# Kernel optimization log

Measured on AMD Instinct MI355X. Metric: run time of the kernel, lower is better.

The kernel has to match this reference:

```python
import jax, jax.numpy as jnp
import numpy as np

D_MODEL = 1024
NUM_HEADS = 16
D_FF = 4096
SEQ = 2048
BATCH = 2
THETA = 10000.0
EPS = 1e-5


def _param(key, shape, fan_in, fan_out):
    std = 2.0 / (fan_in + fan_out) ** 0.5
    return std * jax.random.truncated_normal(key, -3.0, 3.0, shape, dtype=jnp.float32)


def setup_inputs() -> dict:
    key = jax.random.key(0)
    ks = jax.random.split(key, 8)
    d, h, f = D_MODEL, NUM_HEADS, D_FF
    return {
        'x': jax.random.normal(ks[0], (BATCH, SEQ, d), dtype=jnp.float32),
        'token_positions': jnp.arange(SEQ, dtype=jnp.int32),
        'wq': _param(ks[1], (d, d), d, d),
        'wk': _param(ks[2], (d, d), d, d),
        'wv': _param(ks[3], (d, d), d, d),
        'wo': _param(ks[4], (d, d), d, d),
        'ln1_w': jnp.ones((d,), jnp.float32),
        'ln2_w': jnp.ones((d,), jnp.float32),
        'w1': _param(ks[5], (f, d), d, f),
        'w2': _param(ks[6], (d, f), f, d),
        'w3': _param(ks[7], (f, d), d, f),
    }


def rmsnorm(x, w):
    x32 = x.astype(jnp.float32)
    rms = jnp.sqrt(jnp.mean(x32 * x32, axis=-1, keepdims=True) + EPS)
    return ((x32 / rms) * w).astype(x.dtype)


def apply_rope(x, cos, sin):
    # x: [b, h, s, d_k]; cos/sin: [s, d_k//2] -> broadcast as [1,1,s,d_k//2]
    xe, xo = x[..., ::2], x[..., 1::2]
    c = cos[None, None, :, :]
    s = sin[None, None, :, :]
    re = xe * c - xo * s
    ro = xe * s + xo * c
    return jnp.stack((re, ro), axis=-1).reshape(x.shape)


def block_forward(x, token_positions, wq, wk, wv, wo, ln1_w, ln2_w, w1, w2, w3):
    b, s, d = x.shape
    h = NUM_HEADS
    dk = d // h
    # RoPE tables at token positions
    inv_freq = 1.0 / (THETA ** (jnp.arange(0, dk // 2, dtype=jnp.float32) * 2.0 / dk))
    freqs = token_positions.astype(jnp.float32)[:, None] * inv_freq[None, :]  # [s, dk/2]
    cos, sin = jnp.cos(freqs), jnp.sin(freqs)

    # --- attention sublayer (pre-norm) ---
    xn = rmsnorm(x, ln1_w)
    q = jnp.einsum('bsd,ed->bse', xn, wq).reshape(b, s, h, dk).transpose(0, 2, 1, 3)
    k = jnp.einsum('bsd,ed->bse', xn, wk).reshape(b, s, h, dk).transpose(0, 2, 1, 3)
    v = jnp.einsum('bsd,ed->bse', xn, wv).reshape(b, s, h, dk).transpose(0, 2, 1, 3)
    q = apply_rope(q, cos, sin)
    k = apply_rope(k, cos, sin)
    scores = jnp.einsum('bhqd,bhkd->bhqk', q, k) / jnp.sqrt(jnp.float32(dk))
    causal = jnp.tril(jnp.ones((s, s), dtype=bool))
    scores = jnp.where(causal[None, None], scores, -jnp.inf)
    attn = jax.nn.softmax(scores, axis=-1)
    o = jnp.einsum('bhqk,bhkd->bhqd', attn, v)
    o = o.transpose(0, 2, 1, 3).reshape(b, s, d)
    x = x + jnp.einsum('bse,de->bsd', o, wo)

    # --- SwiGLU sublayer (pre-norm) ---
    xn = rmsnorm(x, ln2_w)
    x1 = jnp.einsum('bsd,fd->bsf', xn, w1)
    x3 = jnp.einsum('bsd,fd->bsf', xn, w3)
    gated = (x1 * jax.nn.sigmoid(x1)) * x3
    return x + jnp.einsum('bsf,df->bsd', gated, w2)


def reference(x, token_positions, wq, wk, wv, wo, ln1_w, ln2_w, w1, w2, w3):
    return block_forward(x, token_positions, wq, wk, wv, wo, ln1_w, ln2_w, w1, w2, w3)
```

## Files before the change

### kernel.cpp

```cpp
#include <hip/hip_runtime.h>
#include <hip/hip_bf16.h>

typedef __attribute__((ext_vector_type(4))) float f32x4;
typedef __attribute__((ext_vector_type(8))) short bf16x8;
typedef unsigned short u16;
typedef unsigned int u32;
typedef __attribute__((ext_vector_type(4))) u16 u16x4;

#define DEV static __device__ __forceinline__

constexpr int Bb = 2, Ss = 2048, Dd = 1024, Hh = 16, DKk = 64;
constexpr int Mm = Bb * Ss;

DEV float bf2f(u16 u) { union { u32 i; float f; } v; v.i = (u32)u << 16; return v.f; }
DEV u16 f2bf(float f) {
  union { float f; u32 i; } v; v.f = f;
  u32 r = v.i + 0x7FFFu + ((v.i >> 16) & 1u);
  return (u16)(r >> 16);
}

DEV void gload_lds16(const u16* g, u16* l) {
  __builtin_amdgcn_global_load_lds((const __attribute__((address_space(1))) u32*)g,
                                   (__attribute__((address_space(3))) u32*)l, 16, 0, 0);
}

DEV int swz16(int o) {
  return o ^ (((o >> 8) & 1) << 6) ^ (((o >> 9) & 1) << 5);
}

__global__ void k_cvt_all(const float* __restrict__ wq, const float* __restrict__ wk,
                          const float* __restrict__ wv, const float* __restrict__ wo,
                          const float* __restrict__ w1, const float* __restrict__ w2,
                          const float* __restrict__ w3,
                          u16* __restrict__ wqkv, u16* __restrict__ wob,
                          u16* __restrict__ w13, u16* __restrict__ w2b) {
  int i = (blockIdx.x * 256 + threadIdx.x) * 4;
  int seg = i >> 20;
  const float* src; u16* dst;
  if (seg == 0)      { src = wq + i;             dst = wqkv + i; }
  else if (seg == 1) { src = wk + (i - (1<<20)); dst = wqkv + i; }
  else if (seg == 2) { src = wv + (i - (2<<20)); dst = wqkv + i; }
  else if (seg == 3) { src = wo + (i - (3<<20)); dst = wob  + (i - (3<<20)); }
  else if (seg < 8)  { src = w1 + (i - (4<<20)); dst = w13  + (i - (4<<20)); }
  else if (seg < 12) { src = w2 + (i - (8<<20)); dst = w2b  + (i - (8<<20)); }
  else               { src = w3 + (i - (12<<20)); dst = w13 + (4<<20) + (i - (12<<20)); }
  float4 v = *(const float4*)src;
  u16x4 o = { f2bf(v.x), f2bf(v.y), f2bf(v.z), f2bf(v.w) };
  *(u16x4*)dst = o;
}

__global__ __launch_bounds__(256) void k_rmsnorm(const float* __restrict__ x,
                                                 const float* __restrict__ w,
                                                 u16* __restrict__ out) {
  int row = blockIdx.x;
  int t = threadIdx.x;
  float4 v = ((const float4*)(x + (long)row * Dd))[t];
  float ss = v.x * v.x + v.y * v.y + v.z * v.z + v.w * v.w;
#pragma unroll
  for (int m = 32; m; m >>= 1) ss += __shfl_xor(ss, m, 64);
  __shared__ float red[4];
  if ((t & 63) == 0) red[t >> 6] = ss;
  __syncthreads();
  float tot = red[0] + red[1] + red[2] + red[3];
  float r = rsqrtf(tot * (1.0f / Dd) + 1e-5f);
  float4 wv = ((const float4*)w)[t];
  u16x4 o = { f2bf(v.x * r * wv.x), f2bf(v.y * r * wv.y),
              f2bf(v.z * r * wv.z), f2bf(v.w * r * wv.w) };
  ((u16x4*)(out + (long)row * Dd))[t] = o;
}

__global__ void k_rope(u16* __restrict__ q, u16* __restrict__ k, const int* __restrict__ tp) {
  int idx = blockIdx.x * 256 + threadIdx.x;
  if (idx >= Bb * Ss * Hh * 32) return;
  int p = idx & 31;
  int h = (idx >> 5) & 15;
  int row = idx >> 9;
  int s = row & (Ss - 1);
  float pos = (float)tp[s];
  float invf = __expf(-(float)p * (2.0f / DKk) * 9.2103403719761836f);
  float fr = pos * invf;
  float sn, cs;
  sincosf(fr, &sn, &cs);
  long base = (long)row * Dd + h * DKk + 2 * p;
  float xe = bf2f(q[base]), xo = bf2f(q[base + 1]);
  q[base]     = f2bf((xe * cs - xo * sn) * 0.125f);
  q[base + 1] = f2bf((xe * sn + xo * cs) * 0.125f);
  xe = bf2f(k[base]); xo = bf2f(k[base + 1]);
  k[base]     = f2bf(xe * cs - xo * sn);
  k[base + 1] = f2bf(xe * sn + xo * cs);
}

template <int OM, bool RES>
__global__ __launch_bounds__(256) void k_gemm(const u16* __restrict__ A,
                                              const u16* __restrict__ Bm,
                                              void* __restrict__ Cout,
                                              const float* __restrict__ Rres,
                                              int N, int K) {
  __shared__ u16 Abuf[128 * 32];
  __shared__ u16 Bbuf[128 * 32];
  const int tid = threadIdx.x;
  const int wid = tid >> 6, lane = tid & 63;
  const int wm = wid >> 1, wn = wid & 1;
  const int lq = lane >> 4, ll = lane & 15;
  const int lin = blockIdx.y * gridDim.x + blockIdx.x;
  const int c = lin & 7, j = lin >> 3;
  const int ncc = gridDim.x >> 2;
  const int bxc = (c % ncc) * 4 + (j & 3);
  const int byc = (c / ncc) * 8 + (j >> 2);
  const int m0 = byc * 128, n0 = bxc * 128;

  f32x4 acc[4][4] = {};

  const int srow = tid >> 2;
  const int scol = (tid & 3) * 8;
  const long aoff = (long)(m0 + srow) * K + scol;
  const long boff = (long)(n0 + srow) * K + scol;
  u16* aldsw = Abuf + wid * 512;
  u16* bldsw = Bbuf + wid * 512;

  for (int k0 = 0; k0 < K; k0 += 32) {
    __syncthreads();
    gload_lds16(A + aoff + k0, aldsw);
    gload_lds16(A + aoff + (long)64 * K + k0, aldsw + 2048);
    gload_lds16(Bm + boff + k0, bldsw);
    gload_lds16(Bm + boff + (long)64 * K + k0, bldsw + 2048);
    __syncthreads();
    bf16x8 af[4], bfr[4];
#pragma unroll
    for (int i = 0; i < 4; i++)
      af[i] = *(const bf16x8*)&Abuf[(wm * 64 + i * 16 + ll) * 32 + lq * 8];
#pragma unroll
    for (int j2 = 0; j2 < 4; j2++)
      bfr[j2] = *(const bf16x8*)&Bbuf[(wn * 64 + j2 * 16 + ll) * 32 + lq * 8];
#pragma unroll
    for (int i = 0; i < 4; i++)
#pragma unroll
      for (int j2 = 0; j2 < 4; j2++)
        acc[i][j2] = __builtin_amdgcn_mfma_f32_16x16x32_bf16(af[i], bfr[j2], acc[i][j2], 0, 0, 0);
  }

#pragma unroll
  for (int i = 0; i < 4; i++) {
    const int rowb = m0 + wm * 64 + i * 16 + lq * 4;
#pragma unroll
    for (int j2 = 0; j2 < 4; j2++) {
      const int col = n0 + wn * 64 + j2 * 16 + ll;
#pragma unroll
      for (int r = 0; r < 4; r++) {
        int rr = rowb + r;
        float v = acc[i][j2][r];
        if (RES) v += Rres[(long)rr * N + col];
        if (OM == 1) {
          ((float*)Cout)[(long)rr * N + col] = v;
        } else {
          ((u16*)Cout)[(long)rr * N + col] = f2bf(v);
        }
      }
    }
  }
}

#define STG_A(d, h, kt)                                                         \
  { gload_lds16(A + aoff[0] + (long)(h) * 128 * K + (kt) * 64, &sA[d][h][dst0]); \
    gload_lds16(A + aoff[1] + (long)(h) * 128 * K + (kt) * 64, &sA[d][h][dst1]); }
#define STG_B(d, h, kt)                                                         \
  { gload_lds16(Bp + boff[0] + (long)(h) * 128 * K + (kt) * 64, &sB[d][h][dst0]); \
    gload_lds16(Bp + boff[1] + (long)(h) * 128 * K + (kt) * 64, &sB[d][h][dst1]); }

#define PHASE(q, d, DOB, WVN, ...)                                              \
  {                                                                             \
    bf16x8 af_[2][2];                                                           \
    _Pragma("unroll") for (int s_ = 0; s_ < 2; s_++)                            \
    _Pragma("unroll") for (int kk_ = 0; kk_ < 2; kk_++) {                       \
      int ms_ = (q) * 4 + wm * 2 + s_;                                          \
      int lo_ = ((ms_ & 7) * 16 + ll) * 128 + kk_ * 64 + lq * 16;               \
      af_[s_][kk_] = *(const bf16x8*)((const char*)sA[d][ms_ >> 3] + swz16(lo_)); \
    }                                                                           \
    if (DOB) {                                                                  \
      _Pragma("unroll") for (int ns_ = 0; ns_ < 4; ns_++)                       \
      _Pragma("unroll") for (int kk_ = 0; kk_ < 2; kk_++) {                     \
        int rl_ = wn * 64 + ns_ * 16 + ll;                                      \
        int lo_ = (rl_ & 127) * 128 + kk_ * 64 + lq * 16;                       \
        bfr[ns_][kk_] = *(const bf16x8*)((const char*)sB[d][rl_ >> 7] + swz16(lo_)); \
      }                                                                         \
    }                                                                           \
    __VA_ARGS__;                                                                \
    __builtin_amdgcn_s_barrier();                                               \
    asm volatile("s_waitcnt lgkmcnt(0)" ::: "memory");                          \
    __builtin_amdgcn_sched_barrier(0);                                          \
    __builtin_amdgcn_s_setprio(1);                                              \
    _Pragma("unroll") for (int s_ = 0; s_ < 2; s_++)                            \
    _Pragma("unroll") for (int ns_ = 0; ns_ < 4; ns_++)                         \
    _Pragma("unroll") for (int kk_ = 0; kk_ < 2; kk_++)                         \
      acc[q][s_][ns_] = __builtin_amdgcn_mfma_f32_16x16x32_bf16(                \
          af_[s_][kk_], bfr[ns_][kk_], acc[q][s_][ns_], 0, 0, 0);               \
    __builtin_amdgcn_s_setprio(0);                                              \
    { int wv_ = (WVN);                                                          \
      if (wv_ == 6) { asm volatile("s_waitcnt vmcnt(6)" ::: "memory"); }        \
      else if (wv_ == 0) { asm volatile("s_waitcnt vmcnt(0)" ::: "memory"); } } \
    __builtin_amdgcn_s_barrier();                                               \
  }

template <int OM, int CW, int CH>
__global__ __launch_bounds__(512) void k_gemm8(const u16* __restrict__ A,
                                               const u16* __restrict__ Bm,
                                               void* __restrict__ Cout,
                                               int N, int K) {
  __shared__ u16 sA[2][2][8192];
  __shared__ u16 sB[2][2][8192];
  const int gx = gridDim.x;
  const int lin = blockIdx.y * gx + blockIdx.x;
  const int c = lin & 7, j = lin >> 3;
  const int ncc = gx / CW;
  const int bx = (c % ncc) * CW + j % CW;
  const int by = (c / ncc) * CH + j / CW;
  const long m0 = (long)by * 256, n0 = (long)bx * 256;
  const int tid = threadIdx.x;
  const int wid = tid >> 6, lane = tid & 63;
  const int wm = wid >> 2, wn = wid & 3;
  const int lq = lane >> 4, ll = lane & 15;

  long aoff[2], boff[2];
#pragma unroll
  for (int j2 = 0; j2 < 2; j2++) {
    int off = j2 * 8192 + wid * 1024 + lane * 16;
    int lo = swz16(off);
    int r = lo >> 7, cc = (lo & 127) >> 1;
    aoff[j2] = (m0 + r) * K + cc;
    boff[j2] = (n0 + r) * K + cc;
  }
  const int dst0 = wid * 512;
  const int dst1 = 4096 + wid * 512;

  f32x4 acc[4][2][4];
  bf16x8 bfr[4][2];
  u32 stash[4][2][4][2];

  const int NT = K >> 6;
  const int NI = NT >> 1;
  constexpr int REPS = (OM == 5) ? 2 : 1;

  for (int rep = 0; rep < REPS; rep++) {
    const u16* Bp = Bm + (long)rep * 4096 * K;
    const f32x4 zz = {0.f, 0.f, 0.f, 0.f};
#pragma unroll
    for (int q = 0; q < 4; q++)
#pragma unroll
      for (int s = 0; s < 2; s++)
#pragma unroll
        for (int ns = 0; ns < 4; ns++) acc[q][s][ns] = zz;

    STG_A(0, 0, 0); STG_A(0, 1, 0); STG_B(0, 0, 0); STG_B(0, 1, 0);
    STG_B(1, 0, 1); STG_B(1, 1, 1); STG_A(1, 0, 1);
    asm volatile("s_waitcnt vmcnt(6)" ::: "memory");
    __builtin_amdgcn_s_barrier();

    for (int it = 0; it < NI; it++) {
      const int t = 2 * it;
      const bool full = (t + 2 < NT);
      PHASE(0, 0, true,  -1,            STG_A(1, 1, t + 1))
      PHASE(1, 0, false, -1,            if (full) STG_B(0, 0, t + 2))
      PHASE(2, 0, false, -1,            if (full) STG_B(0, 1, t + 2))
      PHASE(3, 0, false, full ? 6 : 0,  if (full) STG_A(0, 0, t + 2))
      PHASE(0, 1, true,  -1,            if (full) STG_A(0, 1, t + 2))
      PHASE(1, 1, false, -1,            if (full) STG_B(1, 0, t + 3))
      PHASE(2, 1, false, -1,            if (full) STG_B(1, 1, t + 3))
      PHASE(3, 1, false, full ? 6 : -1, if (full) STG_A(1, 0, t + 3))
    }

    if (OM == 5 && rep == 0) {
#pragma unroll
      for (int q = 0; q < 4; q++)
#pragma unroll
        for (int s = 0; s < 2; s++)
#pragma unroll
          for (int ns = 0; ns < 4; ns++) {
            stash[q][s][ns][0] = (u32)f2bf(acc[q][s][ns][0]) | ((u32)f2bf(acc[q][s][ns][1]) << 16);
            stash[q][s][ns][1] = (u32)f2bf(acc[q][s][ns][2]) | ((u32)f2bf(acc[q][s][ns][3]) << 16);
          }
    }
  }

#pragma unroll
  for (int q = 0; q < 4; q++)
#pragma unroll
    for (int s = 0; s < 2; s++) {
      const long row0 = m0 + (q * 4 + wm * 2 + s) * 16 + lq * 4;
#pragma unroll
      for (int ns = 0; ns < 4; ns++) {
        const long col = n0 + wn * 64 + ns * 16 + ll;
#pragma unroll
        for (int r = 0; r < 4; r++) {
          long rr = row0 + r;
          if (OM == 3) {
            float v = acc[q][s][ns][r];
            if (col < 2048) {
              ((u16*)Cout)[(col >> 10) * (long)(Mm * 1024) + rr * 1024 + (col & 1023)] = f2bf(v);
            } else {
              int d = col & 63, hh = ((int)col >> 6) & 15;
              int b2 = (int)rr >> 11, s2 = (int)rr & (Ss - 1);
              ((u16*)Cout)[(long)(2 * Mm * 1024) + ((long)((b2 * Hh + hh) * DKk + d)) * Ss + s2] = f2bf(v);
            }
          } else {
            float v3 = acc[q][s][ns][r];
            u32 st = stash[q][s][ns][r >> 1];
            u16 bb = (r & 1) ? (u16)(st >> 16) : (u16)(st & 0xffffu);
            float v1 = bf2f(bb);
            float g = v1 / (1.0f + __expf(-v1)) * v3;
            ((u16*)Cout)[rr * 4096 + col] = f2bf(g);
          }
        }
      }
    }
}

constexpr int PPAD = 80;

DEV void attn_tile(const u16* __restrict__ Kc, const u16* __restrict__ Vc,
                   u16* __restrict__ myP, const bf16x8* qf, f32x4* accO,
                   float* mrow, float* lrow, int qloc, bool diag, int lq, int ll) {
  f32x4 sacc[4] = {};
#pragma unroll
  for (int fn = 0; fn < 4; fn++)
#pragma unroll
    for (int ks = 0; ks < 2; ks++) {
      bf16x8 kf = *(const bf16x8*)&Kc[(fn * 16 + ll) * 64 + (((ks * 4 + lq) ^ (ll & 7)) * 8)];
      sacc[fn] = __builtin_amdgcn_mfma_f32_16x16x32_bf16(qf[ks], kf, sacc[fn], 0, 0, 0);
    }
  float sv[4][4], pmax[4];
#pragma unroll
  for (int r = 0; r < 4; r++) pmax[r] = -1e30f;
#pragma unroll
  for (int fn = 0; fn < 4; fn++) {
    int kc = fn * 16 + ll;
#pragma unroll
    for (int r = 0; r < 4; r++) {
      float v = sacc[fn][r];
      if (diag && kc > qloc + r) v = -1e30f;
      sv[fn][r] = v;
      pmax[r] = fmaxf(pmax[r], v);
    }
  }
#pragma unroll
  for (int r = 0; r < 4; r++) {
#pragma unroll
    for (int m = 1; m < 16; m <<= 1) pmax[r] = fmaxf(pmax[r], __shfl_xor(pmax[r], m, 64));
  }
  float alpha[4], rsum[4];
#pragma unroll
  for (int r = 0; r < 4; r++) {
    float mnew = fmaxf(mrow[r], pmax[r]);
    alpha[r] = __expf(mrow[r] - mnew);
    mrow[r] = mnew;
    rsum[r] = 0.f;
  }
#pragma unroll
  for (int fn = 0; fn < 4; fn++) {
#pragma unroll
    for (int r = 0; r < 4; r++) {
      float p = __expf(sv[fn][r] - mrow[r]);
      rsum[r] += p;
      myP[(lq * 4 + r) * PPAD + fn * 16 + ll] = f2bf(p);
    }
  }
#pragma unroll
  for (int r = 0; r < 4; r++) {
#pragma unroll
    for (int m = 1; m < 16; m <<= 1) rsum[r] += __shfl_xor(rsum[r], m, 64);
    lrow[r] = lrow[r] * alpha[r] + rsum[r];
  }
#pragma unroll
  for (int fn = 0; fn < 4; fn++)
#pragma unroll
    for (int r = 0; r < 4; r++) accO[fn][r] *= alpha[r];
  bf16x8 pa[2];
#pragma unroll
  for (int ks = 0; ks < 2; ks++)
    pa[ks] = *(const bf16x8*)&myP[ll * PPAD + ks * 32 + lq * 8];
#pragma unroll
  for (int fn = 0; fn < 4; fn++)
#pragma unroll
    for (int ks = 0; ks < 2; ks++) {
      bf16x8 vf = *(const bf16x8*)&Vc[(fn * 16 + ll) * 64 + (((ks * 4 + lq) ^ (ll & 7)) * 8)];
      accO[fn] = __builtin_amdgcn_mfma_f32_16x16x32_bf16(pa[ks], vf, accO[fn], 0, 0, 0);
    }
}

__global__ __launch_bounds__(256) void k_attn(const u16* __restrict__ Q,
                                              const u16* __restrict__ Kb,
                                              const u16* __restrict__ VT,
                                              u16* __restrict__ O) {
  __shared__ u16 Kt[2][64 * 64];
  __shared__ u16 Vt[2][64 * 64];
  __shared__ u16 P[4][16 * PPAD];
  const int pair = blockIdx.x;
  const int bh = blockIdx.y;
  const int b = bh >> 4, h = bh & 15;
  const int tid = threadIdx.x;
  const int wid = tid >> 6, lane = tid & 63;
  const int lq = lane >> 4, ll = lane & 15;
  const int qtA = pair, qtB = 31 - pair;
  const int qr0A = qtA * 64 + wid * 16;
  const int qr0B = qtB * 64 + wid * 16;
  const int qloc = wid * 16 + lq * 4;
  const long qkbase = ((long)b * Ss) * Dd + h * DKk;
  const long vbase  = ((long)(b * Hh + h) * DKk) * Ss;
  const int nk = 32 - pair;

  const int slot0 = wid * 64 + lane;
  const int r0 = slot0 >> 3, c0 = (slot0 & 7) ^ (r0 & 7);
  const int slot1 = 256 + slot0;
  const int r1 = slot1 >> 3, c1 = (slot1 & 7) ^ (r1 & 7);
  const int ldsb0 = (wid * 64) * 8;
  const int ldsb1 = (256 + wid * 64) * 8;

  bf16x8 qfA[2], qfB[2];
#pragma unroll
  for (int ks = 0; ks < 2; ks++) {
    qfA[ks] = *(const bf16x8*)&Q[qkbase + (long)(qr0A + ll) * Dd + ks * 32 + lq * 8];
    qfB[ks] = *(const bf16x8*)&Q[qkbase + (long)(qr0B + ll) * Dd + ks * 32 + lq * 8];
  }

  f32x4 accA[4] = {}, accB[4] = {};
  float mA[4], lA[4], mB[4], lB[4];
#pragma unroll
  for (int r = 0; r < 4; r++) { mA[r] = mB[r] = -1e30f; lA[r] = lB[r] = 0.f; }
  u16* myP = P[wid];

  gload_lds16(Kb + qkbase + (long)r0 * Dd + c0 * 8, Kt[0] + ldsb0);
  gload_lds16(Kb + qkbase + (long)r1 * Dd + c1 * 8, Kt[0] + ldsb1);
  gload_lds16(VT + vbase + (long)r0 * Ss + c0 * 8, Vt[0] + ldsb0);
  gload_lds16(VT + vbase + (long)r1 * Ss + c1 * 8, Vt[0] + ldsb1);
  __syncthreads();

  for (int kt = 0; kt < nk; kt++) {
    if (kt + 1 < nk) {
      const int kn = (kt + 1) * 64;
      u16* kd = Kt[(kt + 1) & 1];
      u16* vd = Vt[(kt + 1) & 1];
      gload_lds16(Kb + qkbase + (long)(kn + r0) * Dd + c0 * 8, kd + ldsb0);
      gload_lds16(Kb + qkbase + (long)(kn + r1) * Dd + c1 * 8, kd + ldsb1);
      gload_lds16(VT + vbase + (long)r0 * Ss + kn + c0 * 8, vd + ldsb0);
      gload_lds16(VT + vbase + (long)r1 * Ss + kn + c1 * 8, vd + ldsb1);
    }
    const u16* Kc = Kt[kt & 1];
    const u16* Vc = Vt[kt & 1];

    attn_tile(Kc, Vc, myP, qfB, accB, mB, lB, qloc, kt == nk - 1, lq, ll);
    if (kt <= pair)
      attn_tile(Kc, Vc, myP, qfA, accA, mA, lA, qloc, kt == pair, lq, ll);
    __syncthreads();
  }

#pragma unroll
  for (int fn = 0; fn < 4; fn++) {
#pragma unroll
    for (int r = 0; r < 4; r++) {
      int rowA = qr0A + lq * 4 + r;
      int rowB = qr0B + lq * 4 + r;
      O[((long)(b * Ss + rowA)) * Dd + h * DKk + fn * 16 + ll] = f2bf(accA[fn][r] / lA[r]);
      O[((long)(b * Ss + rowB)) * Dd + h * DKk + fn * 16 + ll] = f2bf(accB[fn][r] / lB[r]);
    }
  }
}

extern "C" void kernel_launch(void* const* d_in, const int* in_sizes, int n_in,
                              void* d_out, int out_size, void* d_ws, size_t ws_size,
                              hipStream_t stream) {
  const float* x   = (const float*)d_in[0];
  const int*   tp  = (const int*)d_in[1];
  const float* wq  = (const float*)d_in[2];
  const float* wk  = (const float*)d_in[3];
  const float* wv  = (const float*)d_in[4];
  const float* wo  = (const float*)d_in[5];
  const float* ln1 = (const float*)d_in[6];
  const float* ln2 = (const float*)d_in[7];
  const float* w1  = (const float*)d_in[8];
  const float* w2  = (const float*)d_in[9];
  const float* w3  = (const float*)d_in[10];

  char* ws = (char*)d_ws;
  const size_t MB = 1024 * 1024;
  u16*   wqkv_b = (u16*)(ws + 0 * MB);
  u16*   wo_b   = (u16*)(ws + 6 * MB);
  u16*   w13_b  = (u16*)(ws + 8 * MB);
  u16*   w2_b   = (u16*)(ws + 24 * MB);
  u16*   xn     = (u16*)(ws + 32 * MB);
  float* x2     = (float*)(ws + 40 * MB);
  u16*   qb     = (u16*)(ws + 56 * MB);
  u16*   kb     = (u16*)(ws + 64 * MB);
  u16*   vtb    = (u16*)(ws + 72 * MB);
  u16*   ob     = (u16*)(ws + 80 * MB);
  u16*   x1     = (u16*)(ws + 56 * MB);

  k_cvt_all<<<16384, 256, 0, stream>>>(wq, wk, wv, wo, w1, w2, w3,
                                       wqkv_b, wo_b, w13_b, w2_b);
  k_rmsnorm<<<Mm, 256, 0, stream>>>(x, ln1, xn);
  k_gemm8<3, 6, 4><<<dim3(12, 16), 512, 0, stream>>>(xn, wqkv_b, qb, 3072, 1024);
  k_rope<<<(Bb * Ss * Hh * 32) / 256, 256, 0, stream>>>(qb, kb, tp);
  k_attn<<<dim3(16, 32), 256, 0, stream>>>(qb, kb, vtb, ob);
  k_gemm<1, true><<<dim3(8, 32), 256, 0, stream>>>(ob, wo_b, x2, x, 1024, 1024);
  k_rmsnorm<<<Mm, 256, 0, stream>>>(x2, ln2, xn);
  k_gemm8<5, 4, 8><<<dim3(16, 16), 512, 0, stream>>>(xn, w13_b, x1, 4096, 1024);
  k_gemm<1, true><<<dim3(8, 32), 256, 0, stream>>>(x1, w2_b, (float*)d_out, x2, 1024, 4096);
}
```

Before: 380.4 us.

## Unfuse SwiGLU gate from W1/W3 GEMM and split-K the W2 GEMM

```diff
diff --git a/kernel.cpp b/kernel.cpp
--- a/kernel.cpp
+++ b/kernel.cpp
@@ -90,12 +90,36 @@
   k[base + 1] = f2bf(xe * sn + xo * cs);
 }
 
+__global__ void k_gate(u16* __restrict__ x1, const u16* __restrict__ x3, int n) {
+  int i = (blockIdx.x * 256 + threadIdx.x) * 4;
+  if (i >= n) return;
+  u16x4 a = *(u16x4*)(x1 + i);
+  u16x4 b = *(const u16x4*)(x3 + i);
+#pragma unroll
+  for (int j = 0; j < 4; j++) {
+    float v = bf2f(a[j]);
+    float g = v / (1.0f + __expf(-v)) * bf2f(b[j]);
+    a[j] = f2bf(g);
+  }
+  *(u16x4*)(x1 + i) = a;
+}
+
+__global__ void k_addout(const float* __restrict__ p0, const float* __restrict__ p1,
+                         const float* __restrict__ x2, float* __restrict__ out) {
+  int i = (blockIdx.x * 256 + threadIdx.x) * 4;
+  float4 a = *(const float4*)(p0 + i);
+  float4 b = *(const float4*)(p1 + i);
+  float4 c = *(const float4*)(x2 + i);
+  float4 o = { a.x + b.x + c.x, a.y + b.y + c.y, a.z + b.z + c.z, a.w + b.w + c.w };
+  *(float4*)(out + i) = o;
+}
+
 template <int OM, bool RES>
 __global__ __launch_bounds__(256) void k_gemm(const u16* __restrict__ A,
                                               const u16* __restrict__ Bm,
                                               void* __restrict__ Cout,
                                               const float* __restrict__ Rres,
-                                              int N, int K) {
+                                              int N, int Kl, int Kstr) {
   __shared__ u16 Abuf[128 * 32];
   __shared__ u16 Bbuf[128 * 32];
   const int tid = threadIdx.x;
@@ -109,21 +133,24 @@
   const int byc = (c / ncc) * 8 + (j >> 2);
   const int m0 = byc * 128, n0 = bxc * 128;
 
+  const u16* Ap = A + (long)blockIdx.z * Kl;
+  const u16* Bp = Bm + (long)blockIdx.z * Kl;
+
   f32x4 acc[4][4] = {};
 
   const int srow = tid >> 2;
   const int scol = (tid & 3) * 8;
-  const long aoff = (long)(m0 + srow) * K + scol;
-  const long boff = (long)(n0 + srow) * K + scol;
+  const long aoff = (long)(m0 + srow) * Kstr + scol;
+  const long boff = (long)(n0 + srow) * Kstr + scol;
   u16* aldsw = Abuf + wid * 512;
   u16* bldsw = Bbuf + wid * 512;
 
-  for (int k0 = 0; k0 < K; k0 += 32) {
+  for (int k0 = 0; k0 < Kl; k0 += 32) {
     __syncthreads();
-    gload_lds16(A + aoff + k0, aldsw);
-    gload_lds16(A + aoff + (long)64 * K + k0, aldsw + 2048);
-    gload_lds16(Bm + boff + k0, bldsw);
-    gload_lds16(Bm + boff + (long)64 * K + k0, bldsw + 2048);
+    gload_lds16(Ap + aoff + k0, aldsw);
+    gload_lds16(Ap + aoff + (long)64 * Kstr + k0, aldsw + 2048);
+    gload_lds16(Bp + boff + k0, bldsw);
+    gload_lds16(Bp + boff + (long)64 * Kstr + k0, bldsw + 2048);
     __syncthreads();
     bf16x8 af[4], bfr[4];
 #pragma unroll
@@ -139,6 +166,7 @@
         acc[i][j2] = __builtin_amdgcn_mfma_f32_16x16x32_bf16(af[i], bfr[j2], acc[i][j2], 0, 0, 0);
   }
 
+  float* fout = (float*)Cout + (long)blockIdx.z * Mm * (long)N;
 #pragma unroll
   for (int i = 0; i < 4; i++) {
     const int rowb = m0 + wm * 64 + i * 16 + lq * 4;
@@ -151,7 +179,7 @@
         float v = acc[i][j2][r];
         if (RES) v += Rres[(long)rr * N + col];
         if (OM == 1) {
-          ((float*)Cout)[(long)rr * N + col] = v;
+          fout[(long)rr * N + col] = v;
         } else {
           ((u16*)Cout)[(long)rr * N + col] = f2bf(v);
         }
@@ -164,8 +192,8 @@
   { gload_lds16(A + aoff[0] + (long)(h) * 128 * K + (kt) * 64, &sA[d][h][dst0]); \
     gload_lds16(A + aoff[1] + (long)(h) * 128 * K + (kt) * 64, &sA[d][h][dst1]); }
 #define STG_B(d, h, kt)                                                         \
-  { gload_lds16(Bp + boff[0] + (long)(h) * 128 * K + (kt) * 64, &sB[d][h][dst0]); \
-    gload_lds16(Bp + boff[1] + (long)(h) * 128 * K + (kt) * 64, &sB[d][h][dst1]); }
+  { gload_lds16(Bm + boff[0] + (long)(h) * 128 * K + (kt) * 64, &sB[d][h][dst0]); \
+    gload_lds16(Bm + boff[1] + (long)(h) * 128 * K + (kt) * 64, &sB[d][h][dst1]); }
 
 #define PHASE(q, d, DOB, WVN, ...)                                              \
   {                                                                             \
@@ -232,53 +260,28 @@
   const int dst0 = wid * 512;
   const int dst1 = 4096 + wid * 512;
 
-  f32x4 acc[4][2][4];
+  f32x4 acc[4][2][4] = {};
   bf16x8 bfr[4][2];
-  u32 stash[4][2][4][2];
 
   const int NT = K >> 6;
   const int NI = NT >> 1;
-  constexpr int REPS = (OM == 5) ? 2 : 1;
-
-  for (int rep = 0; rep < REPS; rep++) {
-    const u16* Bp = Bm + (long)rep * 4096 * K;
-    const f32x4 zz = {0.f, 0.f, 0.f, 0.f};
-#pragma unroll
-    for (int q = 0; q < 4; q++)
-#pragma unroll
-      for (int s = 0; s < 2; s++)
-#pragma unroll
-        for (int ns = 0; ns < 4; ns++) acc[q][s][ns] = zz;
-
-    STG_A(0, 0, 0); STG_A(0, 1, 0); STG_B(0, 0, 0); STG_B(0, 1, 0);
-    STG_B(1, 0, 1); STG_B(1, 1, 1); STG_A(1, 0, 1);
-    asm volatile("s_waitcnt vmcnt(6)" ::: "memory");
-    __builtin_amdgcn_s_barrier();
-
-    for (int it = 0; it < NI; it++) {
-      const int t = 2 * it;
-      const bool full = (t + 2 < NT);
-      PHASE(0, 0, true,  -1,            STG_A(1, 1, t + 1))
-      PHASE(1, 0, false, -1,            if (full) STG_B(0, 0, t + 2))
-      PHASE(2, 0, false, -1,            if (full) STG_B(0, 1, t + 2))
-      PHASE(3, 0, false, full ? 6 : 0,  if (full) STG_A(0, 0, t + 2))
-      PHASE(0, 1, true,  -1,            if (full) STG_A(0, 1, t + 2))
-      PHASE(1, 1, false, -1,            if (full) STG_B(1, 0, t + 3))
-      PHASE(2, 1, false, -1,            if (full) STG_B(1, 1, t + 3))
-      PHASE(3, 1, false, full ? 6 : -1, if (full) STG_A(1, 0, t + 3))
-    }
-
-    if (OM == 5 && rep == 0) {
-#pragma unroll
-      for (int q = 0; q < 4; q++)
-#pragma unroll
-        for (int s = 0; s < 2; s++)
-#pragma unroll
-          for (int ns = 0; ns < 4; ns++) {
-            stash[q][s][ns][0] = (u32)f2bf(acc[q][s][ns][0]) | ((u32)f2bf(acc[q][s][ns][1]) << 16);
-            stash[q][s][ns][1] = (u32)f2bf(acc[q][s][ns][2]) | ((u32)f2bf(acc[q][s][ns][3]) << 16);
-          }
-    }
+
+  STG_A(0, 0, 0); STG_A(0, 1, 0); STG_B(0, 0, 0); STG_B(0, 1, 0);
+  STG_B(1, 0, 1); STG_B(1, 1, 1); STG_A(1, 0, 1);
+  asm volatile("s_waitcnt vmcnt(6)" ::: "memory");
+  __builtin_amdgcn_s_barrier();
+
+  for (int it = 0; it < NI; it++) {
+    const int t = 2 * it;
+    const bool full = (t + 2 < NT);
+    PHASE(0, 0, true,  -1,            STG_A(1, 1, t + 1))
+    PHASE(1, 0, false, -1,            if (full) STG_B(0, 0, t + 2))
+    PHASE(2, 0, false, -1,            if (full) STG_B(0, 1, t + 2))
+    PHASE(3, 0, false, full ? 6 : 0,  if (full) STG_A(0, 0, t + 2))
+    PHASE(0, 1, true,  -1,            if (full) STG_A(0, 1, t + 2))
+    PHASE(1, 1, false, -1,            if (full) STG_B(1, 0, t + 3))
+    PHASE(2, 1, false, -1,            if (full) STG_B(1, 1, t + 3))
+    PHASE(3, 1, false, full ? 6 : -1, if (full) STG_A(1, 0, t + 3))
   }
 
 #pragma unroll
@@ -291,9 +294,9 @@
         const long col = n0 + wn * 64 + ns * 16 + ll;
 #pragma unroll
         for (int r = 0; r < 4; r++) {
+          float v = acc[q][s][ns][r];
           long rr = row0 + r;
           if (OM == 3) {
-            float v = acc[q][s][ns][r];
             if (col < 2048) {
               ((u16*)Cout)[(col >> 10) * (long)(Mm * 1024) + rr * 1024 + (col & 1023)] = f2bf(v);
             } else {
@@ -302,12 +305,7 @@
               ((u16*)Cout)[(long)(2 * Mm * 1024) + ((long)((b2 * Hh + hh) * DKk + d)) * Ss + s2] = f2bf(v);
             }
           } else {
-            float v3 = acc[q][s][ns][r];
-            u32 st = stash[q][s][ns][r >> 1];
-            u16 bb = (r & 1) ? (u16)(st >> 16) : (u16)(st & 0xffffu);
-            float v1 = bf2f(bb);
-            float g = v1 / (1.0f + __expf(-v1)) * v3;
-            ((u16*)Cout)[rr * 4096 + col] = f2bf(g);
+            ((u16*)Cout)[(col >> 12) * ((long)Mm * 4096) + rr * 4096 + (col & 4095)] = f2bf(v);
           }
         }
       }
@@ -492,6 +490,9 @@
   u16*   vtb    = (u16*)(ws + 72 * MB);
   u16*   ob     = (u16*)(ws + 80 * MB);
   u16*   x1     = (u16*)(ws + 56 * MB);
+  u16*   x3     = (u16*)(ws + 88 * MB);
+  float* p0     = (float*)(ws + 88 * MB);
+  float* p1     = (float*)(ws + 104 * MB);
 
   k_cvt_all<<<16384, 256, 0, stream>>>(wq, wk, wv, wo, w1, w2, w3,
                                        wqkv_b, wo_b, w13_b, w2_b);
@@ -499,8 +500,10 @@
   k_gemm8<3, 6, 4><<<dim3(12, 16), 512, 0, stream>>>(xn, wqkv_b, qb, 3072, 1024);
   k_rope<<<(Bb * Ss * Hh * 32) / 256, 256, 0, stream>>>(qb, kb, tp);
   k_attn<<<dim3(16, 32), 256, 0, stream>>>(qb, kb, vtb, ob);
-  k_gemm<1, true><<<dim3(8, 32), 256, 0, stream>>>(ob, wo_b, x2, x, 1024, 1024);
+  k_gemm<1, true><<<dim3(8, 32), 256, 0, stream>>>(ob, wo_b, x2, x, 1024, 1024, 1024);
   k_rmsnorm<<<Mm, 256, 0, stream>>>(x2, ln2, xn);
-  k_gemm8<5, 4, 8><<<dim3(16, 16), 512, 0, stream>>>(xn, w13_b, x1, 4096, 1024);
-  k_gemm<1, true><<<dim3(8, 32), 256, 0, stream>>>(x1, w2_b, (float*)d_out, x2, 1024, 4096);
-}
+  k_gemm8<4, 4, 8><<<dim3(32, 16), 512, 0, stream>>>(xn, w13_b, x1, 8192, 1024);
+  k_gate<<<16384, 256, 0, stream>>>(x1, x3, 4096 * 4096);
+  k_gemm<1, false><<<dim3(8, 32, 2), 256, 0, stream>>>(x1, w2_b, p0, nullptr, 1024, 2048, 4096);
+  k_addout<<<4096, 256, 0, stream>>>(p0, p1, x2, (float*)d_out);
+}
```

After: 357.5 us. -6.0%, faster.
